# Performance work log

Measured on AMD Instinct MI355X. Metric: run time of the kernel, lower is better.

The kernel has to match this reference:

```python
import jax, jax.numpy as jnp
import numpy as np

B, BEV = 2, 128
Q = BEV * BEV          # 16384 BEV queries
C, H, L, P = 256, 8, 1, 4
D = C // H             # 32 per-head dim


def setup_inputs() -> dict:
    key = jax.random.key(0)
    ks = jax.random.split(key, 14)
    s = 0.02
    return {
        "query": jax.random.normal(ks[0], (B, Q, C), jnp.float32),
        "value": jax.random.normal(ks[1], (B, Q, C), jnp.float32),
        "identity": jax.random.normal(ks[2], (B, Q, C), jnp.float32),
        "query_pos": jax.random.normal(ks[3], (B, Q, C), jnp.float32),
        "reference_points": jax.random.uniform(ks[4], (B, Q, L, 2), jnp.float32),
        "spatial_shapes": jnp.array([[BEV, BEV]], jnp.int32),
        "level_start_index": jnp.array([0], jnp.int32),
        "Wv": jax.random.normal(ks[5], (C, C), jnp.float32) * s,
        "bv": jnp.zeros((C,), jnp.float32),
        "Woff": jax.random.normal(ks[6], (C, H * L * P * 2), jnp.float32) * s,
        "boff": jax.random.normal(ks[7], (H * L * P * 2,), jnp.float32) * s,
        "Ww": jax.random.normal(ks[8], (C, H * L * P), jnp.float32) * s,
        "bw": jnp.zeros((H * L * P,), jnp.float32),
        "Wo": jax.random.normal(ks[9], (C, C), jnp.float32) * s,
        "bo": jnp.zeros((C,), jnp.float32),
    }


def _deform_attn(q, v, reference_points, shapes_np, Wv, bv, Woff, boff, Ww, bw, Wo, bo):
    b, nq, _ = q.shape
    v = v @ Wv + bv                                             # value_proj
    off = (q @ Woff + boff).reshape(b, nq, H, L, P, 2)          # sampling offsets
    attn = jax.nn.softmax((q @ Ww + bw).reshape(b, nq, H, L * P), axis=-1)
    attn = attn.reshape(b, nq, H, L, P)
    # offset normalizer is (W, H) per level
    norm = jnp.asarray(shapes_np[:, ::-1], jnp.float32)         # [L, 2]
    loc = reference_points[:, :, None, :, None, :] + off / norm[None, None, None, :, None, :]

    out = jnp.zeros((b, H, nq, D), jnp.float32)
    start = 0
    for l in range(L):
        Hl, Wl = int(shapes_np[l, 0]), int(shapes_np[l, 1])
        N = Hl * Wl
        vl = v[:, start:start + N].reshape(b, N, H, D).transpose(0, 2, 1, 3)  # [b,H,N,D]
        start += N
        ll = loc[:, :, :, l]                                    # [b,nq,H,P,2] in [0,1]
        # grid_sample(align_corners=False): pixel coord = loc*size - 0.5
        x = ll[..., 0] * Wl - 0.5
        y = ll[..., 1] * Hl - 0.5
        x0 = jnp.floor(x); y0 = jnp.floor(y)
        dx = x - x0; dy = y - y0
        x0i = x0.astype(jnp.int32); y0i = y0.astype(jnp.int32)

        def gather(ix, iy):
            valid = (ix >= 0) & (ix < Wl) & (iy >= 0) & (iy < Hl)  # zero padding
            idx = jnp.clip(iy, 0, Hl - 1) * Wl + jnp.clip(ix, 0, Wl - 1)
            idx = idx.transpose(0, 2, 1, 3).reshape(b, H, nq * P)
            g = jnp.take_along_axis(vl, idx[..., None], axis=2)   # [b,H,nq*P,D]
            return g * valid.transpose(0, 2, 1, 3).reshape(b, H, nq * P, 1)

        def cw(w):  # corner weight -> [b,H,nq*P,1]
            return w.transpose(0, 2, 1, 3).reshape(b, H, nq * P, 1)

        samp = (gather(x0i, y0i) * cw((1 - dx) * (1 - dy))
                + gather(x0i + 1, y0i) * cw(dx * (1 - dy))
                + gather(x0i, y0i + 1) * cw((1 - dx) * dy)
                + gather(x0i + 1, y0i + 1) * cw(dx * dy))
        samp = samp.reshape(b, H, nq, P, D)
        aw = attn[:, :, :, l].transpose(0, 2, 1, 3)             # [b,H,nq,P]
        out = out + jnp.einsum('bhqpd,bhqp->bhqd', samp, aw)

    out = out.transpose(0, 2, 1, 3).reshape(b, nq, C)
    return out @ Wo + bo                                        # output_proj


def reference(query, value, identity, query_pos, reference_points, spatial_shapes,
              level_start_index, Wv, bv, Woff, boff, Ww, bw, Wo, bo):
    shapes_np = np.asarray(spatial_shapes)                      # static level shapes
    q = query + query_pos
    out = _deform_attn(q, value, reference_points, shapes_np,
                       Wv, bv, Woff, boff, Ww, bw, Wo, bo)
    return out + identity
```

## Files before the change

kernel.cpp:

```cpp
#include <hip/hip_runtime.h>
#include <hip/hip_bf16.h>
#include <stdint.h>

#define Q_TOT 32768
#define CC 256
#define GRID_W 128
#define GRID_H 128

typedef __attribute__((ext_vector_type(8))) short short8;
typedef __attribute__((ext_vector_type(4))) float floatx4;

__device__ __forceinline__ ushort f2bf(float f) {
    union { float f; uint32_t u; } v; v.f = f;
    uint32_t r = (v.u + 0x7fffu + ((v.u >> 16) & 1u)) >> 16;
    return (ushort)r;
}
__device__ __forceinline__ float bf2f(ushort s) {
    union { uint32_t u; float f; } v; v.u = ((uint32_t)s) << 16;
    return v.f;
}
__device__ __forceinline__ void bf2x2(uint32_t u, float& lo, float& hi) {
    union { uint32_t u; float f; } a, b;
    a.u = u << 16; b.u = u & 0xffff0000u;
    lo = a.f; hi = b.f;
}
__device__ __forceinline__ void async_load16(const void* g, void* l) {
    __builtin_amdgcn_global_load_lds(
        reinterpret_cast<const __attribute__((address_space(1))) uint32_t*>(
            reinterpret_cast<uintptr_t>(g)),
        reinterpret_cast<__attribute__((address_space(3))) uint32_t*>(
            reinterpret_cast<uintptr_t>(l)),
        16, 0, 0);
}

__global__ __launch_bounds__(256)
void prep_convert(const float* __restrict__ q, const float* __restrict__ qp,
                  const float* __restrict__ val,
                  ushort* __restrict__ qsum, ushort* __restrict__ vbf)
{
    const int total = (Q_TOT * CC) / 4;
    for (int idx = blockIdx.x * blockDim.x + threadIdx.x; idx < 2 * total;
         idx += gridDim.x * blockDim.x) {
        if (idx < total) {
            float4 a = ((const float4*)q)[idx];
            float4 b = ((const float4*)qp)[idx];
            ushort4 o;
            o.x = f2bf(a.x + b.x); o.y = f2bf(a.y + b.y);
            o.z = f2bf(a.z + b.z); o.w = f2bf(a.w + b.w);
            ((ushort4*)qsum)[idx] = o;
        } else {
            int j = idx - total;
            float4 a = ((const float4*)val)[j];
            ushort4 o;
            o.x = f2bf(a.x); o.y = f2bf(a.y); o.z = f2bf(a.z); o.w = f2bf(a.w);
            ((ushort4*)vbf)[j] = o;
        }
    }
}

__global__ __launch_bounds__(256)
void prep_weights(const float* __restrict__ Wv, const float* __restrict__ Wo,
                  const float* __restrict__ Woff, const float* __restrict__ Ww,
                  const float* __restrict__ boff, const float* __restrict__ bw,
                  ushort* __restrict__ WvT, ushort* __restrict__ WoT,
                  ushort* __restrict__ WowT, float* __restrict__ bias_ow)
{
    int idx = blockIdx.x * blockDim.x + threadIdx.x;
    if (idx < 65536) {
        int n = idx >> 8, k = idx & 255;
        WvT[idx] = f2bf(Wv[k * 256 + n]);
    } else if (idx < 131072) {
        int t = idx - 65536; int n = t >> 8, k = t & 255;
        WoT[t] = f2bf(Wo[k * 256 + n]);
    } else if (idx < 155648) {
        int t = idx - 131072; int n = t >> 8, k = t & 255;
        float v = (n < 64) ? Woff[k * 64 + n] : Ww[k * 32 + (n - 64)];
        WowT[t] = f2bf(v);
    } else if (idx < 155744) {
        int t = idx - 155648;
        bias_ow[t] = (t < 64) ? boff[t] : bw[t - 64];
    }
}

template <int BM, int BN, int WAVE_M, int WAVE_N, bool OUT_BF16>
__global__ __launch_bounds__(256)
void gemm_bf16(const ushort* __restrict__ A, const ushort* __restrict__ Bt,
               const float* __restrict__ bias, const float* __restrict__ res,
               void* __restrict__ Cout, int M, int N, int K)
{
    constexpr int TM = BM / WAVE_M / 16;
    constexpr int TN = BN / WAVE_N / 16;
    __shared__ ushort As[BM * 32];
    __shared__ ushort Bs[BN * 32];

    const int tid = threadIdx.x;
    const int lane = tid & 63;
    const int wave = tid >> 6;
    const int wm = wave / WAVE_N;
    const int wn = wave % WAVE_N;
    const int quad = lane >> 4;
    const int m16 = lane & 15;
    const int lrow = lane >> 2;
    const int lkk = (lane & 3) * 8;

    const int row0 = blockIdx.y * BM;
    const int col0 = blockIdx.x * BN;

    floatx4 acc[TM][TN] = {};

    for (int k0 = 0; k0 < K; k0 += 32) {
        #pragma unroll
        for (int i = wave; i < BM / 16; i += 4) {
            const ushort* src = A + (size_t)(row0 + i * 16 + lrow) * K + (k0 + lkk);
            async_load16(src, &As[i * 16 * 32]);
        }
        #pragma unroll
        for (int i = wave; i < BN / 16; i += 4) {
            const ushort* src = Bt + (size_t)(col0 + i * 16 + lrow) * K + (k0 + lkk);
            async_load16(src, &Bs[i * 16 * 32]);
        }
        __syncthreads();

        short8 af[TM], bf[TN];
        #pragma unroll
        for (int i = 0; i < TM; ++i)
            af[i] = *(const short8*)&As[(wm * TM * 16 + i * 16 + m16) * 32 + quad * 8];
        #pragma unroll
        for (int j = 0; j < TN; ++j)
            bf[j] = *(const short8*)&Bs[(wn * TN * 16 + j * 16 + m16) * 32 + quad * 8];
        #pragma unroll
        for (int i = 0; i < TM; ++i)
            #pragma unroll
            for (int j = 0; j < TN; ++j)
                acc[i][j] = __builtin_amdgcn_mfma_f32_16x16x32_bf16(
                    af[i], bf[j], acc[i][j], 0, 0, 0);
        __syncthreads();
    }

    #pragma unroll
    for (int i = 0; i < TM; ++i) {
        #pragma unroll
        for (int j = 0; j < TN; ++j) {
            const int gcol = col0 + wn * TN * 16 + j * 16 + m16;
            const float bb = bias[gcol];
            #pragma unroll
            for (int r = 0; r < 4; ++r) {
                const int grow = row0 + wm * TM * 16 + i * 16 + quad * 4 + r;
                float v = acc[i][j][r] + bb;
                if (res) v += res[(size_t)grow * N + gcol];
                if constexpr (OUT_BF16)
                    ((ushort*)Cout)[(size_t)grow * N + gcol] = f2bf(v);
                else
                    ((float*)Cout)[(size_t)grow * N + gcol] = v;
            }
        }
    }
}

#define QB 8
__global__ __launch_bounds__(256)
void sample_kernel(const ushort* __restrict__ v2,
                   const ushort* __restrict__ ow,
                   const float* __restrict__ ref,
                   ushort* __restrict__ out)
{
    const int tid = threadIdx.x;
    const int ql = tid >> 5;
    const int h  = (tid >> 2) & 7;
    const int dg = tid & 3;
    const int q = blockIdx.x * QB + ql;
    const int b = q >> 14;

    const ushort* op = ow + (size_t)q * 96 + h * 8;
    const uint4 oraw = *(const uint4*)op;
    float offs[8];
    bf2x2(oraw.x, offs[0], offs[1]);
    bf2x2(oraw.y, offs[2], offs[3]);
    bf2x2(oraw.z, offs[4], offs[5]);
    bf2x2(oraw.w, offs[6], offs[7]);

    const uint2 wraw = *(const uint2*)(ow + (size_t)q * 96 + 64 + h * 4);
    float w0, w1, w2, w3;
    bf2x2(wraw.x, w0, w1);
    bf2x2(wraw.y, w2, w3);
    float m = fmaxf(fmaxf(w0, w1), fmaxf(w2, w3));
    float e0 = __expf(w0 - m), e1 = __expf(w1 - m), e2 = __expf(w2 - m), e3 = __expf(w3 - m);
    float inv = 1.f / (e0 + e1 + e2 + e3);
    float aw[4] = {e0 * inv, e1 * inv, e2 * inv, e3 * inv};

    const float rx = ref[(size_t)q * 2 + 0];
    const float ry = ref[(size_t)q * 2 + 1];
    const ushort* vb = v2 + (size_t)b * 16384 * 256 + h * 32 + dg * 8;

    float acc[8] = {};
    #pragma unroll
    for (int p = 0; p < 4; ++p) {
        float x = rx * (float)GRID_W + offs[p * 2 + 0] - 0.5f;
        float y = ry * (float)GRID_H + offs[p * 2 + 1] - 0.5f;
        float x0f = floorf(x), y0f = floorf(y);
        float dx = x - x0f, dy = y - y0f;
        int x0 = (int)x0f, y0 = (int)y0f;
        int x1 = x0 + 1, y1 = y0 + 1;
        float vx0 = (x0 >= 0 && x0 < GRID_W) ? 1.f : 0.f;
        float vx1 = (x1 >= 0 && x1 < GRID_W) ? 1.f : 0.f;
        float vy0 = (y0 >= 0 && y0 < GRID_H) ? 1.f : 0.f;
        float vy1 = (y1 >= 0 && y1 < GRID_H) ? 1.f : 0.f;
        int xc0 = min(max(x0, 0), GRID_W - 1), xc1 = min(max(x1, 0), GRID_W - 1);
        int yc0 = min(max(y0, 0), GRID_H - 1), yc1 = min(max(y1, 0), GRID_H - 1);
        float cw00 = aw[p] * (1.f - dx) * (1.f - dy) * vx0 * vy0;
        float cw10 = aw[p] * dx * (1.f - dy) * vx1 * vy0;
        float cw01 = aw[p] * (1.f - dx) * dy * vx0 * vy1;
        float cw11 = aw[p] * dx * dy * vx1 * vy1;
        const int base0 = yc0 * GRID_W, base1 = yc1 * GRID_W;
        const uint4 r00 = *(const uint4*)(vb + (size_t)(base0 + xc0) * 256);
        const uint4 r10 = *(const uint4*)(vb + (size_t)(base0 + xc1) * 256);
        const uint4 r01 = *(const uint4*)(vb + (size_t)(base1 + xc0) * 256);
        const uint4 r11 = *(const uint4*)(vb + (size_t)(base1 + xc1) * 256);
        float lo, hi;
        bf2x2(r00.x, lo, hi); acc[0] += cw00 * lo; acc[1] += cw00 * hi;
        bf2x2(r00.y, lo, hi); acc[2] += cw00 * lo; acc[3] += cw00 * hi;
        bf2x2(r00.z, lo, hi); acc[4] += cw00 * lo; acc[5] += cw00 * hi;
        bf2x2(r00.w, lo, hi); acc[6] += cw00 * lo; acc[7] += cw00 * hi;
        bf2x2(r10.x, lo, hi); acc[0] += cw10 * lo; acc[1] += cw10 * hi;
        bf2x2(r10.y, lo, hi); acc[2] += cw10 * lo; acc[3] += cw10 * hi;
        bf2x2(r10.z, lo, hi); acc[4] += cw10 * lo; acc[5] += cw10 * hi;
        bf2x2(r10.w, lo, hi); acc[6] += cw10 * lo; acc[7] += cw10 * hi;
        bf2x2(r01.x, lo, hi); acc[0] += cw01 * lo; acc[1] += cw01 * hi;
        bf2x2(r01.y, lo, hi); acc[2] += cw01 * lo; acc[3] += cw01 * hi;
        bf2x2(r01.z, lo, hi); acc[4] += cw01 * lo; acc[5] += cw01 * hi;
        bf2x2(r01.w, lo, hi); acc[6] += cw01 * lo; acc[7] += cw01 * hi;
        bf2x2(r11.x, lo, hi); acc[0] += cw11 * lo; acc[1] += cw11 * hi;
        bf2x2(r11.y, lo, hi); acc[2] += cw11 * lo; acc[3] += cw11 * hi;
        bf2x2(r11.z, lo, hi); acc[4] += cw11 * lo; acc[5] += cw11 * hi;
        bf2x2(r11.w, lo, hi); acc[6] += cw11 * lo; acc[7] += cw11 * hi;
    }

    uint4 o;
    o.x = ((uint32_t)f2bf(acc[1]) << 16) | f2bf(acc[0]);
    o.y = ((uint32_t)f2bf(acc[3]) << 16) | f2bf(acc[2]);
    o.z = ((uint32_t)f2bf(acc[5]) << 16) | f2bf(acc[4]);
    o.w = ((uint32_t)f2bf(acc[7]) << 16) | f2bf(acc[6]);
    *(uint4*)(out + (size_t)q * 256 + h * 32 + dg * 8) = o;
}

extern "C" void kernel_launch(void* const* d_in, const int* in_sizes, int n_in,
                              void* d_out, int out_size, void* d_ws, size_t ws_size,
                              hipStream_t stream) {
    const float* query     = (const float*)d_in[0];
    const float* value     = (const float*)d_in[1];
    const float* identity  = (const float*)d_in[2];
    const float* query_pos = (const float*)d_in[3];
    const float* refpts    = (const float*)d_in[4];
    const float* Wv   = (const float*)d_in[7];
    const float* bv   = (const float*)d_in[8];
    const float* Woff = (const float*)d_in[9];
    const float* boff = (const float*)d_in[10];
    const float* Ww   = (const float*)d_in[11];
    const float* bw   = (const float*)d_in[12];
    const float* Wo   = (const float*)d_in[13];
    const float* bo   = (const float*)d_in[14];
    float* out = (float*)d_out;

    char* ws = (char*)d_ws;
    ushort* qsum_bf  = (ushort*)(ws);
    ushort* value_bf = (ushort*)(ws + 16777216);
    ushort* v2_bf    = (ushort*)(ws + 33554432);
    ushort* ow_bf    = (ushort*)(ws + 50331648);
    ushort* samp_bf  = (ushort*)(ws + 56623104);
    ushort* WvT      = (ushort*)(ws + 73400320);
    ushort* WoT      = (ushort*)(ws + 73531392);
    ushort* WowT     = (ushort*)(ws + 73662464);
    float*  bias_ow  = (float*)(ws + 73711616);

    prep_convert<<<8192, 256, 0, stream>>>(query, query_pos, value, qsum_bf, value_bf);
    prep_weights<<<609, 256, 0, stream>>>(Wv, Wo, Woff, Ww, boff, bw,
                                          WvT, WoT, WowT, bias_ow);
    gemm_bf16<128, 128, 2, 2, true><<<dim3(2, 256), 256, 0, stream>>>(
        value_bf, WvT, bv, nullptr, v2_bf, Q_TOT, 256, 256);
    gemm_bf16<64, 96, 4, 1, true><<<dim3(1, 512), 256, 0, stream>>>(
        qsum_bf, WowT, bias_ow, nullptr, ow_bf, Q_TOT, 96, 256);
    sample_kernel<<<dim3(Q_TOT / QB), 256, 0, stream>>>(v2_bf, ow_bf, refpts, samp_bf);
    gemm_bf16<128, 128, 2, 2, false><<<dim3(2, 256), 256, 0, stream>>>(
        samp_bf, WoT, bo, identity, out, Q_TOT, 256, 256);
}
```

Baseline: 270.1 us.

## Double-buffer GEMM LDS tiles, swizzle workgroup order, shrink GEMM tiles

The bf16 MFMA GEMM now uses two LDS buffers, so the async load for the next K-slice is issued before the MFMAs on the current slice, overlapping global loads with compute. Workgroup IDs are remapped with a stride-8 swizzle, likely aimed at spreading neighbouring tiles across XCDs. The GEMM tile shapes are reduced (128x64, 32x96) to launch more workgroups. The larger LDS footprint and the smaller tiles cost some data reuse and may lower occupancy. With only one barrier per iteration, correctness depends on the async loads having completed before the barrier.

```diff
diff --git a/kernel.cpp b/kernel.cpp
--- a/kernel.cpp
+++ b/kernel.cpp
@@ -90,8 +90,8 @@
 {
     constexpr int TM = BM / WAVE_M / 16;
     constexpr int TN = BN / WAVE_N / 16;
-    __shared__ ushort As[BM * 32];
-    __shared__ ushort Bs[BN * 32];
+    __shared__ ushort As[2][BM * 32];
+    __shared__ ushort Bs[2][BN * 32];
 
     const int tid = threadIdx.x;
     const int lane = tid & 63;
@@ -103,38 +103,53 @@
     const int lrow = lane >> 2;
     const int lkk = (lane & 3) * 8;
 
-    const int row0 = blockIdx.y * BM;
-    const int col0 = blockIdx.x * BN;
+    const int nwg = gridDim.x * gridDim.y;
+    const int hw = blockIdx.y * gridDim.x + blockIdx.x;
+    const int t = (hw & 7) * (nwg >> 3) + (hw >> 3);
+    const int bx = t % gridDim.x;
+    const int by = t / gridDim.x;
+
+    const int row0 = by * BM;
+    const int col0 = bx * BN;
 
     floatx4 acc[TM][TN] = {};
 
-    for (int k0 = 0; k0 < K; k0 += 32) {
+    auto stage = [&](int buf, int k0) {
         #pragma unroll
         for (int i = wave; i < BM / 16; i += 4) {
             const ushort* src = A + (size_t)(row0 + i * 16 + lrow) * K + (k0 + lkk);
-            async_load16(src, &As[i * 16 * 32]);
+            async_load16(src, &As[buf][i * 16 * 32]);
         }
         #pragma unroll
         for (int i = wave; i < BN / 16; i += 4) {
             const ushort* src = Bt + (size_t)(col0 + i * 16 + lrow) * K + (k0 + lkk);
-            async_load16(src, &Bs[i * 16 * 32]);
+            async_load16(src, &Bs[buf][i * 16 * 32]);
         }
-        __syncthreads();
-
-        short8 af[TM], bf[TN];
+    };
+
+    stage(0, 0);
+    __syncthreads();
+
+    int cur = 0;
+    for (int k0 = 0; k0 < K; k0 += 32) {
+        if (k0 + 32 < K) stage(cur ^ 1, k0 + 32);
+
+        short8 af[TM], bfr[TN];
         #pragma unroll
         for (int i = 0; i < TM; ++i)
-            af[i] = *(const short8*)&As[(wm * TM * 16 + i * 16 + m16) * 32 + quad * 8];
+            af[i] = *(const short8*)&As[cur][(wm * TM * 16 + i * 16 + m16) * 32 + quad * 8];
         #pragma unroll
         for (int j = 0; j < TN; ++j)
-            bf[j] = *(const short8*)&Bs[(wn * TN * 16 + j * 16 + m16) * 32 + quad * 8];
+            bfr[j] = *(const short8*)&Bs[cur][(wn * TN * 16 + j * 16 + m16) * 32 + quad * 8];
         #pragma unroll
         for (int i = 0; i < TM; ++i)
             #pragma unroll
             for (int j = 0; j < TN; ++j)
                 acc[i][j] = __builtin_amdgcn_mfma_f32_16x16x32_bf16(
-                    af[i], bf[j], acc[i][j], 0, 0, 0);
+                    af[i], bfr[j], acc[i][j], 0, 0, 0);
+
         __syncthreads();
+        cur ^= 1;
     }
 
     #pragma unroll
@@ -275,11 +290,11 @@
     prep_convert<<<8192, 256, 0, stream>>>(query, query_pos, value, qsum_bf, value_bf);
     prep_weights<<<609, 256, 0, stream>>>(Wv, Wo, Woff, Ww, boff, bw,
                                           WvT, WoT, WowT, bias_ow);
-    gemm_bf16<128, 128, 2, 2, true><<<dim3(2, 256), 256, 0, stream>>>(
+    gemm_bf16<128, 64, 2, 2, true><<<dim3(4, 256), 256, 0, stream>>>(
         value_bf, WvT, bv, nullptr, v2_bf, Q_TOT, 256, 256);
-    gemm_bf16<64, 96, 4, 1, true><<<dim3(1, 512), 256, 0, stream>>>(
+    gemm_bf16<32, 96, 2, 2, true><<<dim3(1, 1024), 256, 0, stream>>>(
         qsum_bf, WowT, bias_ow, nullptr, ow_bf, Q_TOT, 96, 256);
     sample_kernel<<<dim3(Q_TOT / QB), 256, 0, stream>>>(v2_bf, ow_bf, refpts, samp_bf);
-    gemm_bf16<128, 128, 2, 2, false><<<dim3(2, 256), 256, 0, stream>>>(
+    gemm_bf16<128, 64, 2, 2, false><<<dim3(4, 256), 256, 0, stream>>>(
         samp_bf, WoT, bo, identity, out, Q_TOT, 256, 256);
 }
```

New measurement: 257.6 us. 1.05x faster.
